# Performance work log

Hardware: AMD Instinct MI355X
Metric: run time of the kernel (lower is better)

Reference implementation:

```python
import jax, jax.numpy as jnp
import numpy as np

K = 0.15
MOMENTUM = 0.99998
B, C, H, W = 8, 19, 512, 1024


def setup_inputs() -> dict:
    key = jax.random.key(0)
    k1, k2 = jax.random.split(key)
    pred = jax.random.normal(k1, (B, C, H, W), dtype=jnp.float32)
    target = jax.random.randint(k2, (B, H, W), 0, C, dtype=jnp.int32)
    return {"pred": pred, "target": target, "step": 1000}


def reference(pred, target, step):
    b, c, h, w = pred.shape
    # num is a static Python int (step is a Python scalar), matching torch's int(...)
    num = int(K * b * h * w * max(MOMENTUM ** step, K))
    # per-pixel cross entropy, reduction='none': loss[b,h,w] = -log_softmax(pred)[b, target, h, w]
    logp = jax.nn.log_softmax(pred, axis=1)  # [B,C,H,W]
    loss = -jnp.take_along_axis(logp, target[:, None, :, :], axis=1)[:, 0]  # [B,H,W]
    loss = loss.reshape(-1)  # [B*H*W]
    # k-th largest loss value (torch does a full argsort; top_k suffices)
    topv = jax.lax.top_k(loss, num)[0]
    TK = topv[num - 1]
    mask = loss >= TK  # includes ties, like torch's boolean indexing
    return jnp.sum(jnp.where(mask, loss, 0.0)) / jnp.sum(mask).astype(loss.dtype)
```

## Files before the change

### kernel.cpp

```cpp
#include <hip/hip_runtime.h>

#define BB 8
#define CCH 19
#define HH 512
#define WW 1024
#define HW (HH * WW)
#define NPIX (BB * HW)
#define CHW (CCH * HW)
#define N4 (NPIX / 4)

#define FIX_SCALE 17179869184.0

struct SelState {
    unsigned num;
    unsigned b1, k1;
};

__device__ __forceinline__ unsigned fkey(float x) {
    unsigned u = __float_as_uint(x);
    return (u & 0x80000000u) ? ~u : (u | 0x80000000u);
}

__device__ __forceinline__ unsigned long long fix64(float x) {
    return (unsigned long long)(long long)((double)x * FIX_SCALE);
}

__global__ __launch_bounds__(256) void k_init(const int* __restrict__ step_p,
                                              unsigned* __restrict__ zbase,
                                              SelState* st) {
    for (int i = threadIdx.x; i < 8448; i += 256) zbase[i] = 0u;
    __syncthreads();
    if (threadIdx.x == 0) {
        int step = step_p[0];
        double m = pow(0.99998, (double)step);
        double Kc = 0.15;
        double f = m > Kc ? m : Kc;
        st->num = (unsigned)(Kc * (double)BB * (double)HH * (double)WW * f);
    }
}

__global__ __launch_bounds__(256) void k_loss_hist(const float* __restrict__ pred,
                                                   const int* __restrict__ target,
                                                   float* __restrict__ loss,
                                                   unsigned* __restrict__ hist) {
    __shared__ unsigned h[2048];
    for (int i = threadIdx.x; i < 2048; i += 256) h[i] = 0;
    __syncthreads();

    int stride = gridDim.x * 256;
    for (int i4 = blockIdx.x * 256 + threadIdx.x; i4 < N4; i4 += stride) {
        int p0 = i4 << 2;
        int b = p0 >> 19;
        int hw = p0 & (HW - 1);
        const float* base = pred + (size_t)b * CHW + hw;

        float4 v[CCH];
#pragma unroll
        for (int c = 0; c < CCH; ++c)
            v[c] = *reinterpret_cast<const float4*>(base + (size_t)c * HW);
        int4 tg = *reinterpret_cast<const int4*>(target + p0);

        float4 mx = v[0];
#pragma unroll
        for (int c = 1; c < CCH; ++c) {
            mx.x = fmaxf(mx.x, v[c].x);
            mx.y = fmaxf(mx.y, v[c].y);
            mx.z = fmaxf(mx.z, v[c].z);
            mx.w = fmaxf(mx.w, v[c].w);
        }
        float4 s = make_float4(0.f, 0.f, 0.f, 0.f);
        float4 xt = make_float4(0.f, 0.f, 0.f, 0.f);
#pragma unroll
        for (int c = 0; c < CCH; ++c) {
            s.x += __expf(v[c].x - mx.x);
            s.y += __expf(v[c].y - mx.y);
            s.z += __expf(v[c].z - mx.z);
            s.w += __expf(v[c].w - mx.w);
            xt.x = (tg.x == c) ? v[c].x : xt.x;
            xt.y = (tg.y == c) ? v[c].y : xt.y;
            xt.z = (tg.z == c) ? v[c].z : xt.z;
            xt.w = (tg.w == c) ? v[c].w : xt.w;
        }
        float4 o;
        o.x = __logf(s.x) + mx.x - xt.x;
        o.y = __logf(s.y) + mx.y - xt.y;
        o.z = __logf(s.z) + mx.z - xt.z;
        o.w = __logf(s.w) + mx.w - xt.w;
        *reinterpret_cast<float4*>(loss + p0) = o;

        atomicAdd(&h[fkey(o.x) >> 21], 1u);
        atomicAdd(&h[fkey(o.y) >> 21], 1u);
        atomicAdd(&h[fkey(o.z) >> 21], 1u);
        atomicAdd(&h[fkey(o.w) >> 21], 1u);
    }
    __syncthreads();
    for (int i = threadIdx.x; i < 2048; i += 256) {
        unsigned c = h[i];
        if (c) atomicAdd(&hist[i], c);
    }
}

__global__ __launch_bounds__(256) void k_scan1(const unsigned* __restrict__ hist,
                                               SelState* st) {
    __shared__ unsigned chunk[256];
    int t = threadIdx.x;
    unsigned k = st->num;

    unsigned local[8];
    unsigned lsum = 0;
#pragma unroll
    for (int j = 0; j < 8; ++j) { local[j] = hist[t * 8 + j]; lsum += local[j]; }
    chunk[t] = lsum;
    __syncthreads();
    for (int off = 1; off < 256; off <<= 1) {
        unsigned add = (t + off < 256) ? chunk[t + off] : 0u;
        __syncthreads();
        chunk[t] += add;
        __syncthreads();
    }
    unsigned cum = (t < 255) ? chunk[t + 1] : 0u;
#pragma unroll
    for (int j = 7; j >= 0; --j) {
        unsigned c = local[j];
        if (k > cum && k <= cum + c) {
            st->b1 = (unsigned)(t * 8 + j);
            st->k1 = k - cum;
        }
        cum += c;
    }
}

__global__ __launch_bounds__(256) void k_hist2(const float* __restrict__ loss,
                                               const SelState* __restrict__ st,
                                               unsigned* __restrict__ h2g,
                                               unsigned long long* __restrict__ bs2g,
                                               unsigned long long* __restrict__ aboveSum,
                                               unsigned* __restrict__ aboveCnt) {
    __shared__ unsigned h[2048];
    __shared__ unsigned long long bs[2048];
    for (int i = threadIdx.x; i < 2048; i += 256) { h[i] = 0; bs[i] = 0ull; }
    __syncthreads();
    unsigned b1 = st->b1;
    unsigned long long asum = 0ull;
    unsigned acnt = 0;
    int stride = gridDim.x * 256;
    for (int i4 = blockIdx.x * 256 + threadIdx.x; i4 < N4; i4 += stride) {
        float4 v = reinterpret_cast<const float4*>(loss)[i4];
        unsigned u, hi;
        u = fkey(v.x); hi = u >> 21;
        if (hi > b1) { asum += fix64(v.x); acnt++; }
        else if (hi == b1) { unsigned idx = (u >> 10) & 2047u; atomicAdd(&h[idx], 1u); atomicAdd(&bs[idx], fix64(v.x)); }
        u = fkey(v.y); hi = u >> 21;
        if (hi > b1) { asum += fix64(v.y); acnt++; }
        else if (hi == b1) { unsigned idx = (u >> 10) & 2047u; atomicAdd(&h[idx], 1u); atomicAdd(&bs[idx], fix64(v.y)); }
        u = fkey(v.z); hi = u >> 21;
        if (hi > b1) { asum += fix64(v.z); acnt++; }
        else if (hi == b1) { unsigned idx = (u >> 10) & 2047u; atomicAdd(&h[idx], 1u); atomicAdd(&bs[idx], fix64(v.z)); }
        u = fkey(v.w); hi = u >> 21;
        if (hi > b1) { asum += fix64(v.w); acnt++; }
        else if (hi == b1) { unsigned idx = (u >> 10) & 2047u; atomicAdd(&h[idx], 1u); atomicAdd(&bs[idx], fix64(v.w)); }
    }
#pragma unroll
    for (int off = 32; off >= 1; off >>= 1) {
        asum += __shfl_down(asum, off);
        acnt += __shfl_down(acnt, off);
    }
    __shared__ unsigned long long wsum[4];
    __shared__ unsigned wcnt[4];
    int wid = threadIdx.x >> 6, lane = threadIdx.x & 63;
    if (lane == 0) { wsum[wid] = asum; wcnt[wid] = acnt; }
    __syncthreads();
    if (threadIdx.x == 0) {
        unsigned long long ts = wsum[0] + wsum[1] + wsum[2] + wsum[3];
        unsigned tc = wcnt[0] + wcnt[1] + wcnt[2] + wcnt[3];
        if (ts) atomicAdd(aboveSum, ts);
        if (tc) atomicAdd(aboveCnt, tc);
    }
    __syncthreads();
    for (int i = threadIdx.x; i < 2048; i += 256) {
        unsigned c = h[i];
        if (c) { atomicAdd(&h2g[i], c); atomicAdd(&bs2g[i], bs[i]); }
    }
}

__global__ __launch_bounds__(256) void k_last(const unsigned* __restrict__ h2,
                                              const unsigned long long* __restrict__ bs2,
                                              const unsigned long long* __restrict__ aboveSum,
                                              const unsigned* __restrict__ aboveCnt,
                                              const SelState* __restrict__ st,
                                              float* __restrict__ out) {
    __shared__ unsigned chunk[256];
    __shared__ unsigned b2sh;
    __shared__ unsigned long long wsum[4];
    __shared__ unsigned wcnt[4];
    int t = threadIdx.x;
    unsigned k = st->k1;
    if (t == 0) b2sh = 0u;

    unsigned local[8];
    unsigned lsum = 0;
#pragma unroll
    for (int j = 0; j < 8; ++j) { local[j] = h2[t * 8 + j]; lsum += local[j]; }
    chunk[t] = lsum;
    __syncthreads();
    for (int off = 1; off < 256; off <<= 1) {
        unsigned add = (t + off < 256) ? chunk[t + off] : 0u;
        __syncthreads();
        chunk[t] += add;
        __syncthreads();
    }
    unsigned cum = (t < 255) ? chunk[t + 1] : 0u;
#pragma unroll
    for (int j = 7; j >= 0; --j) {
        unsigned c = local[j];
        if (k > cum && k <= cum + c) b2sh = (unsigned)(t * 8 + j);
        cum += c;
    }
    __syncthreads();
    unsigned b2 = b2sh;

    unsigned long long s = 0ull;
    unsigned cnt = 0;
#pragma unroll
    for (int j = 0; j < 8; ++j) {
        unsigned bin = (unsigned)(t * 8 + j);
        if (bin >= b2) { s += bs2[bin]; cnt += local[j]; }
    }
#pragma unroll
    for (int off = 32; off >= 1; off >>= 1) {
        s += __shfl_down(s, off);
        cnt += __shfl_down(cnt, off);
    }
    int wid = t >> 6, lane = t & 63;
    if (lane == 0) { wsum[wid] = s; wcnt[wid] = cnt; }
    __syncthreads();
    if (t == 0) {
        unsigned long long ts = wsum[0] + wsum[1] + wsum[2] + wsum[3] + aboveSum[0];
        unsigned long long tc = (unsigned long long)(wcnt[0] + wcnt[1] + wcnt[2] + wcnt[3])
                              + (unsigned long long)aboveCnt[0];
        long long ss = (long long)ts;
        out[0] = (float)(((double)ss / FIX_SCALE) / (double)tc);
    }
}

extern "C" void kernel_launch(void* const* d_in, const int* in_sizes, int n_in,
                              void* d_out, int out_size, void* d_ws, size_t ws_size,
                              hipStream_t stream) {
    const float* pred = (const float*)d_in[0];
    const int* target = (const int*)d_in[1];
    const int* step = (const int*)d_in[2];
    float* out = (float*)d_out;

    char* ws = (char*)d_ws;
    const size_t LOSS_BYTES = (size_t)NPIX * 4;
    float* loss = (float*)ws;
    char* sb = ws + LOSS_BYTES;
    unsigned* h1 = (unsigned*)(sb);
    unsigned* h2 = (unsigned*)(sb + 8192);
    unsigned long long* bs2 = (unsigned long long*)(sb + 16384);
    unsigned long long* aboveSum = (unsigned long long*)(sb + 32768);
    unsigned* aboveCnt = (unsigned*)(sb + 32776);
    SelState* st = (SelState*)(sb + 32784);

    k_init<<<1, 256, 0, stream>>>(step, h1, st);
    k_loss_hist<<<1024, 256, 0, stream>>>(pred, target, loss, h1);
    k_scan1<<<1, 256, 0, stream>>>(h1, st);
    k_hist2<<<1024, 256, 0, stream>>>(loss, st, h2, bs2, aboveSum, aboveCnt);
    k_last<<<1, 256, 0, stream>>>(h2, bs2, aboveSum, aboveCnt, st, out);
}
```

Before: 115.7 us.

## Fuse scan and finalize into last-block tails; drop max-subtraction in softmax

Cuts the five-launch pipeline to a memset plus two grid kernels. A last-block ticket in each grid kernel now runs the histogram scan and the final reduction, and the init kernel is replaced by hipMemsetAsync. The loss kernel no longer subtracts the per-pixel max before exp, which saves a pass but can overflow for large logits. It also uses nontemporal loads for pred and a fixed 4-iteration unrolled loop, which adds launch-free tails and relies on the grid size dividing the work exactly.

Result: slower. 326.6 us (+182.3%).

```diff
diff --git a/kernel.cpp b/kernel.cpp
--- a/kernel.cpp
+++ b/kernel.cpp
@@ -8,11 +8,14 @@
 #define NPIX (BB * HW)
 #define CHW (CCH * HW)
 #define N4 (NPIX / 4)
+#define GRID 1024
+#define BLOCK 256
 
 #define FIX_SCALE 17179869184.0
 
+typedef float f32x4 __attribute__((ext_vector_type(4)));
+
 struct SelState {
-    unsigned num;
     unsigned b1, k1;
 };
 
@@ -20,132 +23,127 @@
     unsigned u = __float_as_uint(x);
     return (u & 0x80000000u) ? ~u : (u | 0x80000000u);
 }
-
 __device__ __forceinline__ unsigned long long fix64(float x) {
     return (unsigned long long)(long long)((double)x * FIX_SCALE);
 }
-
-__global__ __launch_bounds__(256) void k_init(const int* __restrict__ step_p,
-                                              unsigned* __restrict__ zbase,
-                                              SelState* st) {
-    for (int i = threadIdx.x; i < 8448; i += 256) zbase[i] = 0u;
-    __syncthreads();
-    if (threadIdx.x == 0) {
-        int step = step_p[0];
-        double m = pow(0.99998, (double)step);
-        double Kc = 0.15;
-        double f = m > Kc ? m : Kc;
-        st->num = (unsigned)(Kc * (double)BB * (double)HH * (double)WW * f);
-    }
-}
-
-__global__ __launch_bounds__(256) void k_loss_hist(const float* __restrict__ pred,
-                                                   const int* __restrict__ target,
-                                                   float* __restrict__ loss,
-                                                   unsigned* __restrict__ hist) {
+__device__ __forceinline__ unsigned agent_load_u32(const unsigned* p) {
+    return __hip_atomic_load(p, __ATOMIC_RELAXED, __HIP_MEMORY_SCOPE_AGENT);
+}
+__device__ __forceinline__ unsigned long long agent_load_u64(const unsigned long long* p) {
+    return __hip_atomic_load(p, __ATOMIC_RELAXED, __HIP_MEMORY_SCOPE_AGENT);
+}
+
+__global__ __launch_bounds__(BLOCK) void k1_loss_hist(
+    const float* __restrict__ pred, const int* __restrict__ target,
+    const int* __restrict__ step_p, float* __restrict__ loss,
+    unsigned* __restrict__ h1, SelState* __restrict__ st,
+    unsigned* __restrict__ ticket)
+{
     __shared__ unsigned h[2048];
-    for (int i = threadIdx.x; i < 2048; i += 256) h[i] = 0;
-    __syncthreads();
-
-    int stride = gridDim.x * 256;
-    for (int i4 = blockIdx.x * 256 + threadIdx.x; i4 < N4; i4 += stride) {
-        int p0 = i4 << 2;
-        int b = p0 >> 19;
-        int hw = p0 & (HW - 1);
+    __shared__ unsigned chunk[256];
+    __shared__ unsigned isLast;
+    const int tid = threadIdx.x, bid = blockIdx.x;
+
+    for (int i = tid; i < 2048; i += BLOCK) h[i] = 0u;
+    __syncthreads();
+
+#pragma unroll
+    for (int it = 0; it < 4; ++it) {
+        const int i4 = (bid * BLOCK + tid) + it * (GRID * BLOCK);
+        const int p0 = i4 << 2;
+        const int b = p0 >> 19;
+        const int hw = p0 & (HW - 1);
         const float* base = pred + (size_t)b * CHW + hw;
-
-        float4 v[CCH];
-#pragma unroll
-        for (int c = 0; c < CCH; ++c)
-            v[c] = *reinterpret_cast<const float4*>(base + (size_t)c * HW);
-        int4 tg = *reinterpret_cast<const int4*>(target + p0);
-
-        float4 mx = v[0];
-#pragma unroll
-        for (int c = 1; c < CCH; ++c) {
-            mx.x = fmaxf(mx.x, v[c].x);
-            mx.y = fmaxf(mx.y, v[c].y);
-            mx.z = fmaxf(mx.z, v[c].z);
-            mx.w = fmaxf(mx.w, v[c].w);
+        const int4 tg = *reinterpret_cast<const int4*>(target + p0);
+        float sx = 0.f, sy = 0.f, sz = 0.f, sw = 0.f;
+        float xx = 0.f, xy = 0.f, xz = 0.f, xw = 0.f;
+#pragma unroll
+        for (int c = 0; c < CCH; ++c) {
+            const f32x4 v = __builtin_nontemporal_load(
+                reinterpret_cast<const f32x4*>(base + (size_t)c * HW));
+            sx += __expf(v.x); sy += __expf(v.y);
+            sz += __expf(v.z); sw += __expf(v.w);
+            xx = (tg.x == c) ? v.x : xx;
+            xy = (tg.y == c) ? v.y : xy;
+            xz = (tg.z == c) ? v.z : xz;
+            xw = (tg.w == c) ? v.w : xw;
         }
-        float4 s = make_float4(0.f, 0.f, 0.f, 0.f);
-        float4 xt = make_float4(0.f, 0.f, 0.f, 0.f);
-#pragma unroll
-        for (int c = 0; c < CCH; ++c) {
-            s.x += __expf(v[c].x - mx.x);
-            s.y += __expf(v[c].y - mx.y);
-            s.z += __expf(v[c].z - mx.z);
-            s.w += __expf(v[c].w - mx.w);
-            xt.x = (tg.x == c) ? v[c].x : xt.x;
-            xt.y = (tg.y == c) ? v[c].y : xt.y;
-            xt.z = (tg.z == c) ? v[c].z : xt.z;
-            xt.w = (tg.w == c) ? v[c].w : xt.w;
-        }
-        float4 o;
-        o.x = __logf(s.x) + mx.x - xt.x;
-        o.y = __logf(s.y) + mx.y - xt.y;
-        o.z = __logf(s.z) + mx.z - xt.z;
-        o.w = __logf(s.w) + mx.w - xt.w;
-        *reinterpret_cast<float4*>(loss + p0) = o;
-
+        f32x4 o;
+        o.x = __logf(sx) - xx;
+        o.y = __logf(sy) - xy;
+        o.z = __logf(sz) - xz;
+        o.w = __logf(sw) - xw;
+        *reinterpret_cast<f32x4*>(loss + p0) = o;
         atomicAdd(&h[fkey(o.x) >> 21], 1u);
         atomicAdd(&h[fkey(o.y) >> 21], 1u);
         atomicAdd(&h[fkey(o.z) >> 21], 1u);
         atomicAdd(&h[fkey(o.w) >> 21], 1u);
     }
     __syncthreads();
-    for (int i = threadIdx.x; i < 2048; i += 256) {
+    for (int i = tid; i < 2048; i += BLOCK) {
         unsigned c = h[i];
-        if (c) atomicAdd(&hist[i], c);
-    }
-}
-
-__global__ __launch_bounds__(256) void k_scan1(const unsigned* __restrict__ hist,
-                                               SelState* st) {
-    __shared__ unsigned chunk[256];
-    int t = threadIdx.x;
-    unsigned k = st->num;
-
+        if (c) atomicAdd(&h1[i], c);
+    }
+    __threadfence();
+    if (tid == 0) isLast = (atomicAdd(ticket, 1u) == GRID - 1) ? 1u : 0u;
+    __syncthreads();
+    if (!isLast) return;
+
+    unsigned num;
+    {
+        int s = step_p[0];
+        double m = pow(0.99998, (double)s);
+        double f = m > 0.15 ? m : 0.15;
+        num = (unsigned)(0.15 * (double)BB * (double)HH * (double)WW * f);
+    }
     unsigned local[8];
     unsigned lsum = 0;
 #pragma unroll
-    for (int j = 0; j < 8; ++j) { local[j] = hist[t * 8 + j]; lsum += local[j]; }
-    chunk[t] = lsum;
+    for (int j = 0; j < 8; ++j) { local[j] = agent_load_u32(&h1[tid * 8 + j]); lsum += local[j]; }
+    chunk[tid] = lsum;
     __syncthreads();
     for (int off = 1; off < 256; off <<= 1) {
-        unsigned add = (t + off < 256) ? chunk[t + off] : 0u;
-        __syncthreads();
-        chunk[t] += add;
-        __syncthreads();
-    }
-    unsigned cum = (t < 255) ? chunk[t + 1] : 0u;
+        unsigned add = (tid + off < 256) ? chunk[tid + off] : 0u;
+        __syncthreads();
+        chunk[tid] += add;
+        __syncthreads();
+    }
+    unsigned cum = (tid < 255) ? chunk[tid + 1] : 0u;
 #pragma unroll
     for (int j = 7; j >= 0; --j) {
         unsigned c = local[j];
-        if (k > cum && k <= cum + c) {
-            st->b1 = (unsigned)(t * 8 + j);
-            st->k1 = k - cum;
+        if (num > cum && num <= cum + c) {
+            st->b1 = (unsigned)(tid * 8 + j);
+            st->k1 = num - cum;
         }
         cum += c;
     }
 }
 
-__global__ __launch_bounds__(256) void k_hist2(const float* __restrict__ loss,
-                                               const SelState* __restrict__ st,
-                                               unsigned* __restrict__ h2g,
-                                               unsigned long long* __restrict__ bs2g,
-                                               unsigned long long* __restrict__ aboveSum,
-                                               unsigned* __restrict__ aboveCnt) {
+__global__ __launch_bounds__(BLOCK) void k2_select(
+    const float* __restrict__ loss, const SelState* __restrict__ st,
+    unsigned* __restrict__ h2, unsigned long long* __restrict__ bs2,
+    unsigned long long* __restrict__ aboveSum, unsigned* __restrict__ aboveCnt,
+    unsigned* __restrict__ ticket, float* __restrict__ out)
+{
     __shared__ unsigned h[2048];
     __shared__ unsigned long long bs[2048];
-    for (int i = threadIdx.x; i < 2048; i += 256) { h[i] = 0; bs[i] = 0ull; }
-    __syncthreads();
-    unsigned b1 = st->b1;
+    __shared__ unsigned chunk[256];
+    __shared__ unsigned b_sh, isLast;
+    __shared__ unsigned long long wsum[4];
+    __shared__ unsigned wcnt[4];
+    const int tid = threadIdx.x, bid = blockIdx.x;
+
+    for (int i = tid; i < 2048; i += BLOCK) { h[i] = 0u; bs[i] = 0ull; }
+    __syncthreads();
+
+    const unsigned b1 = st->b1;
     unsigned long long asum = 0ull;
     unsigned acnt = 0;
-    int stride = gridDim.x * 256;
-    for (int i4 = blockIdx.x * 256 + threadIdx.x; i4 < N4; i4 += stride) {
-        float4 v = reinterpret_cast<const float4*>(loss)[i4];
+#pragma unroll
+    for (int it = 0; it < 4; ++it) {
+        const int i4 = (bid * BLOCK + tid) + it * (GRID * BLOCK);
+        const f32x4 v = reinterpret_cast<const f32x4*>(loss)[i4];
         unsigned u, hi;
         u = fkey(v.x); hi = u >> 21;
         if (hi > b1) { asum += fix64(v.x); acnt++; }
@@ -165,81 +163,75 @@
         asum += __shfl_down(asum, off);
         acnt += __shfl_down(acnt, off);
     }
-    __shared__ unsigned long long wsum[4];
-    __shared__ unsigned wcnt[4];
-    int wid = threadIdx.x >> 6, lane = threadIdx.x & 63;
-    if (lane == 0) { wsum[wid] = asum; wcnt[wid] = acnt; }
-    __syncthreads();
-    if (threadIdx.x == 0) {
+    {
+        const int wid = tid >> 6, lane = tid & 63;
+        if (lane == 0) { wsum[wid] = asum; wcnt[wid] = acnt; }
+    }
+    __syncthreads();
+    if (tid == 0) {
         unsigned long long ts = wsum[0] + wsum[1] + wsum[2] + wsum[3];
         unsigned tc = wcnt[0] + wcnt[1] + wcnt[2] + wcnt[3];
         if (ts) atomicAdd(aboveSum, ts);
         if (tc) atomicAdd(aboveCnt, tc);
     }
     __syncthreads();
-    for (int i = threadIdx.x; i < 2048; i += 256) {
+    for (int i = tid; i < 2048; i += BLOCK) {
         unsigned c = h[i];
-        if (c) { atomicAdd(&h2g[i], c); atomicAdd(&bs2g[i], bs[i]); }
-    }
-}
-
-__global__ __launch_bounds__(256) void k_last(const unsigned* __restrict__ h2,
-                                              const unsigned long long* __restrict__ bs2,
-                                              const unsigned long long* __restrict__ aboveSum,
-                                              const unsigned* __restrict__ aboveCnt,
-                                              const SelState* __restrict__ st,
-                                              float* __restrict__ out) {
-    __shared__ unsigned chunk[256];
-    __shared__ unsigned b2sh;
-    __shared__ unsigned long long wsum[4];
-    __shared__ unsigned wcnt[4];
-    int t = threadIdx.x;
-    unsigned k = st->k1;
-    if (t == 0) b2sh = 0u;
-
+        if (c) { atomicAdd(&h2[i], c); atomicAdd(&bs2[i], bs[i]); }
+    }
+    __threadfence();
+    if (tid == 0) isLast = (atomicAdd(ticket, 1u) == GRID - 1) ? 1u : 0u;
+    __syncthreads();
+    if (!isLast) return;
+
+    const unsigned k1 = st->k1;
+    if (tid == 0) b_sh = 0u;
     unsigned local[8];
     unsigned lsum = 0;
 #pragma unroll
-    for (int j = 0; j < 8; ++j) { local[j] = h2[t * 8 + j]; lsum += local[j]; }
-    chunk[t] = lsum;
+    for (int j = 0; j < 8; ++j) { local[j] = agent_load_u32(&h2[tid * 8 + j]); lsum += local[j]; }
+    chunk[tid] = lsum;
     __syncthreads();
     for (int off = 1; off < 256; off <<= 1) {
-        unsigned add = (t + off < 256) ? chunk[t + off] : 0u;
-        __syncthreads();
-        chunk[t] += add;
-        __syncthreads();
-    }
-    unsigned cum = (t < 255) ? chunk[t + 1] : 0u;
-#pragma unroll
-    for (int j = 7; j >= 0; --j) {
-        unsigned c = local[j];
-        if (k > cum && k <= cum + c) b2sh = (unsigned)(t * 8 + j);
-        cum += c;
-    }
-    __syncthreads();
-    unsigned b2 = b2sh;
+        unsigned add = (tid + off < 256) ? chunk[tid + off] : 0u;
+        __syncthreads();
+        chunk[tid] += add;
+        __syncthreads();
+    }
+    {
+        unsigned cum = (tid < 255) ? chunk[tid + 1] : 0u;
+#pragma unroll
+        for (int j = 7; j >= 0; --j) {
+            unsigned c = local[j];
+            if (k1 > cum && k1 <= cum + c) b_sh = (unsigned)(tid * 8 + j);
+            cum += c;
+        }
+    }
+    __syncthreads();
+    const unsigned b2 = b_sh;
 
     unsigned long long s = 0ull;
     unsigned cnt = 0;
 #pragma unroll
     for (int j = 0; j < 8; ++j) {
-        unsigned bin = (unsigned)(t * 8 + j);
-        if (bin >= b2) { s += bs2[bin]; cnt += local[j]; }
+        const unsigned bin = (unsigned)(tid * 8 + j);
+        if (bin >= b2) { s += agent_load_u64(&bs2[bin]); cnt += local[j]; }
     }
 #pragma unroll
     for (int off = 32; off >= 1; off >>= 1) {
         s += __shfl_down(s, off);
         cnt += __shfl_down(cnt, off);
     }
-    int wid = t >> 6, lane = t & 63;
-    if (lane == 0) { wsum[wid] = s; wcnt[wid] = cnt; }
-    __syncthreads();
-    if (t == 0) {
-        unsigned long long ts = wsum[0] + wsum[1] + wsum[2] + wsum[3] + aboveSum[0];
+    {
+        const int wid = tid >> 6, lane = tid & 63;
+        if (lane == 0) { wsum[wid] = s; wcnt[wid] = cnt; }
+    }
+    __syncthreads();
+    if (tid == 0) {
+        unsigned long long ts = wsum[0] + wsum[1] + wsum[2] + wsum[3] + agent_load_u64(aboveSum);
         unsigned long long tc = (unsigned long long)(wcnt[0] + wcnt[1] + wcnt[2] + wcnt[3])
-                              + (unsigned long long)aboveCnt[0];
-        long long ss = (long long)ts;
-        out[0] = (float)(((double)ss / FIX_SCALE) / (double)tc);
+                              + (unsigned long long)agent_load_u32(aboveCnt);
+        out[0] = (float)(((double)(long long)ts / FIX_SCALE) / (double)tc);
     }
 }
 
@@ -260,11 +252,11 @@
     unsigned long long* bs2 = (unsigned long long*)(sb + 16384);
     unsigned long long* aboveSum = (unsigned long long*)(sb + 32768);
     unsigned* aboveCnt = (unsigned*)(sb + 32776);
-    SelState* st = (SelState*)(sb + 32784);
-
-    k_init<<<1, 256, 0, stream>>>(step, h1, st);
-    k_loss_hist<<<1024, 256, 0, stream>>>(pred, target, loss, h1);
-    k_scan1<<<1, 256, 0, stream>>>(h1, st);
-    k_hist2<<<1024, 256, 0, stream>>>(loss, st, h2, bs2, aboveSum, aboveCnt);
-    k_last<<<1, 256, 0, stream>>>(h2, bs2, aboveSum, aboveCnt, st, out);
-}
+    unsigned* ticket1 = (unsigned*)(sb + 32780);
+    unsigned* ticket2 = (unsigned*)(sb + 32784);
+    SelState* st = (SelState*)(sb + 32792);
+
+    hipMemsetAsync(sb, 0, 32788, stream);
+    k1_loss_hist<<<GRID, BLOCK, 0, stream>>>(pred, target, step, loss, h1, st, ticket1);
+    k2_select<<<GRID, BLOCK, 0, stream>>>(loss, st, h2, bs2, aboveSum, aboveCnt, ticket2, out);
+}
```
